# Kernel tuning notes

Measured on AMD Instinct MI355X. Metric: run time of the kernel, lower is better.

Reference implementation:

```python
import jax, jax.numpy as jnp
import numpy as np

# Dimensions
BATCH, L, DM = 4, 2048, 768          # batch, seq_len, d_model
EXPAND, DS, DC = 2, 16, 4            # expand, d_state, d_conv (mamba defaults)
DI = EXPAND * DM                     # d_inner = 1536
DTR = DM // 16                       # dt_rank = 48


def setup_inputs() -> dict:
    key = jax.random.key(0)
    ks = jax.random.split(key, 8)
    g = lambda k, shp, s=0.02: (jax.random.normal(k, shp, jnp.float32) * s)
    inputs = {
        "input": jax.random.normal(ks[0], (BATCH, L, DM), jnp.float32),
        "ln_w": jnp.ones((DM,), jnp.float32),
        "ln_b": jnp.zeros((DM,), jnp.float32),
        "W_in": g(ks[1], (2 * DI, DM)),            # in_proj weight (no bias)
        "conv_w": g(ks[2], (DI, 1, DC), 0.1),      # depthwise causal conv
        "conv_b": jnp.zeros((DI,), jnp.float32),
        "W_x": g(ks[3], (DTR + 2 * DS, DI)),       # x_proj -> (dt, B, C)
        "W_dt": g(ks[4], (DI, DTR)),               # dt_proj weight
        "b_dt": jnp.full((DI,), -4.0, jnp.float32),# dt_proj bias (small init dt)
        "A_log": jnp.log(jnp.broadcast_to(jnp.arange(1, DS + 1, dtype=jnp.float32), (DI, DS))),
        "D_ssm": jnp.ones((DI,), jnp.float32),
        "W_out": g(ks[5], (DM, DI)),               # out_proj (no bias)
    }
    return inputs


def _mamba_forward(input, ln_w, ln_b, W_in, conv_w, conv_b, W_x, W_dt, b_dt, A_log, D_ssm, W_out):
    skip = input
    # LayerNorm over last dim
    mu = jnp.mean(input, axis=-1, keepdims=True)
    var = jnp.var(input, axis=-1, keepdims=True)
    xn = (input - mu) * jax.lax.rsqrt(var + 1e-5) * ln_w + ln_b

    # in_proj -> x, z  (B, L, 2*DI)
    xz = jnp.einsum("bld,ed->ble", xn, W_in)
    x, z = jnp.split(xz, 2, axis=-1)

    # depthwise causal conv1d along L, then SiLU
    xc = jnp.transpose(x, (0, 2, 1))  # (B, DI, L)
    xc = jax.lax.conv_general_dilated(
        xc, conv_w, window_strides=(1,), padding=[(DC - 1, 0)],
        feature_group_count=conv_w.shape[0],
        dimension_numbers=("NCH", "OIH", "NCH"))
    xc = xc + conv_b[None, :, None]
    u = jax.nn.silu(jnp.transpose(xc, (0, 2, 1)))  # (B, L, DI)

    # x_proj -> dt, Bmat, Cmat
    dbc = jnp.einsum("bld,ed->ble", u, W_x)
    dt_rank = W_dt.shape[1]
    d_state = A_log.shape[1]
    dt = dbc[..., :dt_rank]
    Bm = dbc[..., dt_rank:dt_rank + d_state]   # (B, L, DS)
    Cm = dbc[..., dt_rank + d_state:]          # (B, L, DS)

    delta = jax.nn.softplus(jnp.einsum("blr,dr->bld", dt, W_dt) + b_dt)  # (B, L, DI)
    A = -jnp.exp(A_log)  # (DI, DS)

    def step(h, inp):
        d_t, B_t, C_t, u_t = inp  # (B,DI),(B,DS),(B,DS),(B,DI)
        dA = jnp.exp(d_t[..., None] * A)                       # (B, DI, DS)
        h = dA * h + (d_t * u_t)[..., None] * B_t[:, None, :]  # (B, DI, DS)
        y_t = jnp.einsum("bds,bs->bd", h, C_t)
        return h, y_t

    h0 = jnp.zeros((u.shape[0], A.shape[0], d_state), u.dtype)
    xs = (jnp.swapaxes(delta, 0, 1), jnp.swapaxes(Bm, 0, 1),
          jnp.swapaxes(Cm, 0, 1), jnp.swapaxes(u, 0, 1))
    _, ys = jax.lax.scan(step, h0, xs)
    y = jnp.swapaxes(ys, 0, 1) + u * D_ssm  # (B, L, DI)

    y = y * jax.nn.silu(z)
    out = jnp.einsum("ble,de->bld", y, W_out)
    return out + skip


def reference(input, ln_w, ln_b, W_in, conv_w, conv_b, W_x, W_dt, b_dt, A_log, D_ssm, W_out):
    return _mamba_forward(input, ln_w, ln_b, W_in, conv_w, conv_b, W_x, W_dt, b_dt, A_log, D_ssm, W_out)
```

## Files before the change

### kernel.cpp

```cpp
#include <hip/hip_runtime.h>
#include <math.h>

#define BATCH 4
#define SEQL  2048
#define DM    768
#define DI    1536
#define DS    16
#define DTR   48
#define NXZ   3072
#define NDBC  80
#define MROWS (BATCH*SEQL)
#define CHUNK 32
#define NC    (SEQL/CHUNK)

typedef __bf16 bf16x8 __attribute__((ext_vector_type(8)));
typedef float  f32x4  __attribute__((ext_vector_type(4)));
typedef float  f32x2  __attribute__((ext_vector_type(2)));
typedef unsigned short u16x8 __attribute__((ext_vector_type(8)));

__device__ __forceinline__ unsigned short f2bf(float f) {
    unsigned int u = __float_as_uint(f);
    unsigned int r = u + 0x7fffu + ((u >> 16) & 1u);
    return (unsigned short)(r >> 16);
}
__device__ __forceinline__ float bf2f(unsigned short u) {
    return __uint_as_float((unsigned int)u << 16);
}

__device__ __forceinline__ void gload16(const unsigned short* g, unsigned short* l) {
    __builtin_amdgcn_global_load_lds(
        (const __attribute__((address_space(1))) unsigned int*)g,
        (__attribute__((address_space(3))) unsigned int*)l,
        16, 0, 0);
}

#define VM_WAIT(n) asm volatile("s_waitcnt vmcnt(" #n ")" ::: "memory")
#define LGKM_WAIT0() asm volatile("s_waitcnt lgkmcnt(0)" ::: "memory")
#define RAW_BAR() asm volatile("s_barrier" ::: "memory")

__global__ __launch_bounds__(256) void convert_all(const float* __restrict__ W_in,
                                                   const float* __restrict__ W_x,
                                                   const float* __restrict__ W_out,
                                                   const float* __restrict__ W_dt,
                                                   unsigned short* __restrict__ Win_bf,
                                                   unsigned short* __restrict__ Wx_bf,
                                                   unsigned short* __restrict__ Wout_bf,
                                                   unsigned short* __restrict__ Wdt_bf)
{
    int bid = blockIdx.x, tid = threadIdx.x;
    const float* in; unsigned short* out; int i;
    if (bid < 2304)      { in = W_in;  out = Win_bf;  i = bid * 256 + tid;          if (i >= 589824) return; }
    else if (bid < 2424) { in = W_x;   out = Wx_bf;   i = (bid - 2304) * 256 + tid; if (i >= 30720)  return; }
    else if (bid < 3576) { in = W_out; out = Wout_bf; i = (bid - 2424) * 256 + tid; if (i >= 294912) return; }
    else {
        int j = (bid - 3576) * 256 + tid;
        int n = j >> 6, k = j & 63;
        Wdt_bf[j] = (k < 48) ? f2bf(W_dt[n * 48 + k]) : (unsigned short)0;
        return;
    }
    float4 v = *reinterpret_cast<const float4*>(in + (size_t)i * 4);
    size_t o = (size_t)i * 4;
    out[o+0] = f2bf(v.x); out[o+1] = f2bf(v.y);
    out[o+2] = f2bf(v.z); out[o+3] = f2bf(v.w);
}

__global__ __launch_bounds__(192) void ln_kernel(const float* __restrict__ inp,
                                                 const float* __restrict__ w,
                                                 const float* __restrict__ b,
                                                 unsigned short* __restrict__ out)
{
    int row = blockIdx.x;
    const float* x = inp + (size_t)row * DM;
    unsigned short* o = out + (size_t)row * DM;
    int tid = threadIdx.x;

    float4 v = *reinterpret_cast<const float4*>(x + tid * 4);
    float s  = v.x + v.y + v.z + v.w;
    float sq = v.x*v.x + v.y*v.y + v.z*v.z + v.w*v.w;

    for (int off = 32; off > 0; off >>= 1) {
        s  += __shfl_down(s, off);
        sq += __shfl_down(sq, off);
    }
    __shared__ float sa[3], sb[3];
    int lane = tid & 63, wv = tid >> 6;
    if (lane == 0) { sa[wv] = s; sb[wv] = sq; }
    __syncthreads();
    float tot  = sa[0] + sa[1] + sa[2];
    float totq = sb[0] + sb[1] + sb[2];

    float mean = tot * (1.0f / DM);
    float var  = totq * (1.0f / DM) - mean * mean;
    float rstd = rsqrtf(var + 1e-5f);

    float4 wv4 = *reinterpret_cast<const float4*>(w + tid * 4);
    float4 bv4 = *reinterpret_cast<const float4*>(b + tid * 4);
    ushort4 o4;
    o4.x = f2bf((v.x - mean) * rstd * wv4.x + bv4.x);
    o4.y = f2bf((v.y - mean) * rstd * wv4.y + bv4.y);
    o4.z = f2bf((v.z - mean) * rstd * wv4.z + bv4.z);
    o4.w = f2bf((v.w - mean) * rstd * wv4.w + bv4.w);
    *reinterpret_cast<ushort4*>(o + tid * 4) = o4;
}

__global__ __launch_bounds__(512, 2) void gemm_256(const unsigned short* __restrict__ A,
                                                   const unsigned short* __restrict__ W,
                                                   unsigned short* __restrict__ C, int ldc,
                                                   int K)
{
    extern __shared__ unsigned short smem[];
    unsigned short* As0 = smem;
    unsigned short* Bs0 = smem + 2 * 16384;

    const int tid  = threadIdx.x;
    const int lane = tid & 63;
    const int w    = tid >> 6;
    const int wm   = w >> 2, wn = w & 3;

    const int flat = blockIdx.y * gridDim.x + blockIdx.x;
    const int cpx  = (gridDim.x * gridDim.y) >> 3;
    const int swz  = (flat & 7) * cpx + (flat >> 3);
    const int m0   = (swz / gridDim.x) * 256;
    const int n0   = (swz % gridDim.x) * 256;

    const int rq = lane >> 3;
    const int cbk = (lane & 7) ^ rq;
    const unsigned short* pA[4];
    const unsigned short* pB[4];
    #pragma unroll
    for (int i = 0; i < 4; ++i) {
        int row = (w * 4 + i) * 8 + rq;
        pA[i] = A + (size_t)(m0 + row) * K + cbk * 8;
        pB[i] = W + (size_t)(n0 + row) * K + cbk * 8;
    }

    const int lr  = lane & 15;
    const int ln4 = lane >> 4;

    f32x4 acc[8][4];
    #pragma unroll
    for (int f = 0; f < 8; ++f)
        #pragma unroll
        for (int g = 0; g < 4; ++g)
            acc[f][g] = (f32x4){0.f, 0.f, 0.f, 0.f};

    const int NT = K >> 6;

    auto STAGE = [&](int bufi, int kt) {
        #pragma unroll
        for (int i = 0; i < 4; ++i) {
            gload16(pA[i] + (size_t)kt * 64, &As0[bufi * 16384 + (w * 4 + i) * 512]);
            gload16(pB[i] + (size_t)kt * 64, &Bs0[bufi * 16384 + (w * 4 + i) * 512]);
        }
    };

    STAGE(0, 0);
    VM_WAIT(0);
    RAW_BAR();
    STAGE(1, 1);

    int cur = 0;
    for (int kt = 0; kt < NT; ++kt) {
        const unsigned short* Ab = &As0[cur * 16384];
        const unsigned short* Bb = &Bs0[cur * 16384];
        #pragma unroll
        for (int kk = 0; kk < 2; ++kk) {
            const int co = ((kk * 4 + ln4) ^ (lr & 7)) * 8;
            bf16x8 af[8], bfr[4];
            #pragma unroll
            for (int f = 0; f < 8; ++f)
                af[f] = *reinterpret_cast<const bf16x8*>(&Ab[(wm * 128 + f * 16 + lr) * 64 + co]);
            #pragma unroll
            for (int g = 0; g < 4; ++g)
                bfr[g] = *reinterpret_cast<const bf16x8*>(&Bb[(wn * 64 + g * 16 + lr) * 64 + co]);
            __builtin_amdgcn_s_setprio(1);
            #pragma unroll
            for (int f = 0; f < 8; ++f)
                #pragma unroll
                for (int g = 0; g < 4; ++g)
                    acc[f][g] = __builtin_amdgcn_mfma_f32_16x16x32_bf16(af[f], bfr[g], acc[f][g], 0, 0, 0);
            __builtin_amdgcn_s_setprio(0);
        }

        if (kt + 1 < NT) {
            LGKM_WAIT0();
            RAW_BAR();
            if (kt + 2 < NT) {
                STAGE(cur, kt + 2);
                VM_WAIT(8);
            } else {
                VM_WAIT(0);
            }
            RAW_BAR();
            cur ^= 1;
        }
    }

    const int cr = ln4 * 4;
    #pragma unroll
    for (int f = 0; f < 8; ++f) {
        int mbase = m0 + wm * 128 + f * 16 + cr;
        #pragma unroll
        for (int g = 0; g < 4; ++g) {
            int n = n0 + wn * 64 + g * 16 + lr;
            #pragma unroll
            for (int r = 0; r < 4; ++r)
                C[(size_t)(mbase + r) * ldc + n] = f2bf(acc[f][g][r]);
        }
    }
}

template<int EPI>
__global__ __launch_bounds__(256) void gemm_pipe(const unsigned short* __restrict__ A,
                                                 const unsigned short* __restrict__ W,
                                                 void* __restrict__ Cv, int ldc,
                                                 int K,
                                                 const float* __restrict__ skip)
{
    __shared__ unsigned short As[2][128 * 64];
    __shared__ unsigned short Bs[2][128 * 64];

    const int tid  = threadIdx.x;
    const int lane = tid & 63;
    const int wid  = tid >> 6;
    const int wr   = wid >> 1, wcn = wid & 1;

    const int flat = blockIdx.y * gridDim.x + blockIdx.x;
    const int cpx  = (gridDim.x * gridDim.y) >> 3;
    const int swz  = (flat & 7) * cpx + (flat >> 3);
    const int m0   = (swz / gridDim.x) * 128;
    const int n0   = (swz % gridDim.x) * 128;

    const int swz3 = (tid >> 3) & 7;
    const unsigned short* pA = A + (size_t)(m0 + (tid >> 3)) * K + ((tid & 7) ^ swz3) * 8;
    const unsigned short* pB = W + (size_t)(n0 + (tid >> 3)) * K + ((tid & 7) ^ swz3) * 8;

    const int lr   = lane & 15;
    const int ln4  = lane >> 4;
    const int swzA = lr & 7;
    const int aoff = (wr * 64 + lr) * 64;
    const int boff = (wcn * 64 + lr) * 64;
    const int co0  = (ln4 ^ swzA) * 8;
    const int co1  = ((4 + ln4) ^ swzA) * 8;

    f32x4 acc[4][4];
    #pragma unroll
    for (int i = 0; i < 4; ++i)
        #pragma unroll
        for (int j = 0; j < 4; ++j)
            acc[i][j] = (f32x4){0.f, 0.f, 0.f, 0.f};

    const int NT = K >> 6;

    auto STAGE = [&](int bufi, int kt) {
        const unsigned short* a = pA + (size_t)kt * 64;
        const unsigned short* b = pB + (size_t)kt * 64;
        #pragma unroll
        for (int i = 0; i < 4; ++i) {
            gload16(a + (size_t)i * 32 * K, &As[bufi][(i * 256 + wid * 64) * 8]);
            gload16(b + (size_t)i * 32 * K, &Bs[bufi][(i * 256 + wid * 64) * 8]);
        }
    };

    STAGE(0, 0);
    VM_WAIT(0);
    RAW_BAR();
    STAGE(1, 1);

    int cur = 0;
    for (int kt = 0; kt < NT; ++kt) {
        const unsigned short* Ab = &As[cur][0];
        const unsigned short* Bb = &Bs[cur][0];
        #pragma unroll
        for (int kk = 0; kk < 2; ++kk) {
            const int co = kk ? co1 : co0;
            bf16x8 af[4], bfr[4];
            #pragma unroll
            for (int i = 0; i < 4; ++i)
                af[i] = *reinterpret_cast<const bf16x8*>(&Ab[aoff + i * 1024 + co]);
            #pragma unroll
            for (int j = 0; j < 4; ++j)
                bfr[j] = *reinterpret_cast<const bf16x8*>(&Bb[boff + j * 1024 + co]);
            #pragma unroll
            for (int i = 0; i < 4; ++i)
                #pragma unroll
                for (int j = 0; j < 4; ++j)
                    acc[i][j] = __builtin_amdgcn_mfma_f32_16x16x32_bf16(af[i], bfr[j], acc[i][j], 0, 0, 0);
        }

        if (kt + 1 < NT) {
            LGKM_WAIT0();
            RAW_BAR();
            if (kt + 2 < NT) {
                STAGE(cur, kt + 2);
                VM_WAIT(8);
            } else {
                VM_WAIT(0);
            }
            RAW_BAR();
            cur ^= 1;
        }
    }

    const int cr = ln4 * 4, cc = lr;
    #pragma unroll
    for (int i = 0; i < 4; ++i) {
        int mbase = m0 + wr * 64 + i * 16 + cr;
        #pragma unroll
        for (int j = 0; j < 4; ++j) {
            int n = n0 + wcn * 64 + j * 16 + cc;
            #pragma unroll
            for (int r = 0; r < 4; ++r) {
                float v = acc[i][j][r];
                size_t off = (size_t)(mbase + r) * ldc + n;
                if constexpr (EPI == 0) {
                    ((unsigned short*)Cv)[off] = f2bf(v);
                } else {
                    ((float*)Cv)[off] = v + skip[off];
                }
            }
        }
    }
}

__global__ __launch_bounds__(256) void gemm_k64_sp(const unsigned short* __restrict__ A,
                                                   const unsigned short* __restrict__ W,
                                                   unsigned short* __restrict__ C,
                                                   const float* __restrict__ bias)
{
    __shared__ unsigned short As[128 * 64];
    __shared__ unsigned short Bs[128 * 64];

    const int tid  = threadIdx.x;
    const int lane = tid & 63;
    const int wid  = tid >> 6;
    const int wr   = wid >> 1, wcn = wid & 1;

    const int flat = blockIdx.y * gridDim.x + blockIdx.x;
    const int cpx  = (gridDim.x * gridDim.y) >> 3;
    const int swz  = (flat & 7) * cpx + (flat >> 3);
    const int m0   = (swz / gridDim.x) * 128;
    const int n0   = (swz % gridDim.x) * 128;

    const int swz3 = (tid >> 3) & 7;
    const unsigned short* pA = A + (size_t)(m0 + (tid >> 3)) * 64 + ((tid & 7) ^ swz3) * 8;
    const unsigned short* pB = W + (size_t)(n0 + (tid >> 3)) * 64 + ((tid & 7) ^ swz3) * 8;

    #pragma unroll
    for (int i = 0; i < 4; ++i) {
        gload16(pA + (size_t)i * 32 * 64, &As[(i * 256 + wid * 64) * 8]);
        gload16(pB + (size_t)i * 32 * 64, &Bs[(i * 256 + wid * 64) * 8]);
    }
    __syncthreads();

    const int lr   = lane & 15;
    const int ln4  = lane >> 4;
    const int swzA = lr & 7;
    const int aoff = (wr * 64 + lr) * 64;
    const int boff = (wcn * 64 + lr) * 64;
    const int co0  = (ln4 ^ swzA) * 8;
    const int co1  = ((4 + ln4) ^ swzA) * 8;

    f32x4 acc[4][4];
    #pragma unroll
    for (int i = 0; i < 4; ++i)
        #pragma unroll
        for (int j = 0; j < 4; ++j)
            acc[i][j] = (f32x4){0.f, 0.f, 0.f, 0.f};

    #pragma unroll
    for (int kk = 0; kk < 2; ++kk) {
        const int co = kk ? co1 : co0;
        bf16x8 af[4], bfr[4];
        #pragma unroll
        for (int i = 0; i < 4; ++i)
            af[i] = *reinterpret_cast<const bf16x8*>(&As[aoff + i * 1024 + co]);
        #pragma unroll
        for (int j = 0; j < 4; ++j)
            bfr[j] = *reinterpret_cast<const bf16x8*>(&Bs[boff + j * 1024 + co]);
        #pragma unroll
        for (int i = 0; i < 4; ++i)
            #pragma unroll
            for (int j = 0; j < 4; ++j)
                acc[i][j] = __builtin_amdgcn_mfma_f32_16x16x32_bf16(af[i], bfr[j], acc[i][j], 0, 0, 0);
    }

    const int cr = ln4 * 4, cc = lr;
    #pragma unroll
    for (int i = 0; i < 4; ++i) {
        int mbase = m0 + wr * 64 + i * 16 + cr;
        #pragma unroll
        for (int j = 0; j < 4; ++j) {
            int n = n0 + wcn * 64 + j * 16 + cc;
            float bb = bias[n];
            #pragma unroll
            for (int r = 0; r < 4; ++r) {
                float v = acc[i][j][r] + bb;
                v = (v > 20.f) ? v : log1pf(__expf(v));
                C[(size_t)(mbase + r) * DI + n] = f2bf(v);
            }
        }
    }
}

#define KS 384
__global__ __launch_bounds__(256) void gemm_dbc_k4(const unsigned short* __restrict__ A,
                                                   const unsigned short* __restrict__ W,
                                                   float* __restrict__ part)
{
    __shared__ unsigned short As[128 * 32];
    __shared__ unsigned short Bs[128 * 32];

    const int tid  = threadIdx.x;
    const int lane = tid & 63;
    const int w    = tid >> 6;
    const int wr   = w >> 1, wc = w & 1;
    const int kx   = blockIdx.x;
    const int m0   = blockIdx.y * 128;

    const int srow = tid >> 2;
    const int scb  = (tid & 3) ^ ((srow >> 1) & 3);
    const unsigned short* Ap0 = A + (size_t)(m0 + srow) * DI + kx * KS + scb * 8;
    const unsigned short* Ap1 = Ap0 + (size_t)64 * DI;
    int br0 = min(srow, NDBC - 1);
    int br1 = min(64 + srow, NDBC - 1);
    const unsigned short* Wp0 = W + (size_t)br0 * DI + kx * KS + scb * 8;
    const unsigned short* Wp1 = W + (size_t)br1 * DI + kx * KS + scb * 8;

    f32x4 acc[4][4];
    #pragma unroll
    for (int i = 0; i < 4; ++i)
        #pragma unroll
        for (int j = 0; j < 4; ++j)
            acc[i][j] = (f32x4){0.f, 0.f, 0.f, 0.f};

    const int lr = lane & 15;
    const int lk = (((lane >> 4) ^ ((lr >> 1) & 3))) * 8;

    for (int k0 = 0; k0 < KS; k0 += 32) {
        gload16(Ap0 + k0, &As[0] + w * 512);
        gload16(Ap1 + k0, &As[0] + 2048 + w * 512);
        gload16(Wp0 + k0, &Bs[0] + w * 512);
        gload16(Wp1 + k0, &Bs[0] + 2048 + w * 512);
        __syncthreads();

        bf16x8 af[4], bfr[4];
        #pragma unroll
        for (int i = 0; i < 4; ++i)
            af[i] = *reinterpret_cast<const bf16x8*>(&As[(wr*64 + i*16 + lr) * 32 + lk]);
        #pragma unroll
        for (int j = 0; j < 4; ++j)
            bfr[j] = *reinterpret_cast<const bf16x8*>(&Bs[(wc*64 + j*16 + lr) * 32 + lk]);

        #pragma unroll
        for (int i = 0; i < 4; ++i)
            #pragma unroll
            for (int j = 0; j < 4; ++j)
                acc[i][j] = __builtin_amdgcn_mfma_f32_16x16x32_bf16(af[i], bfr[j], acc[i][j], 0, 0, 0);
        __syncthreads();
    }

    const int cr = (lane >> 4) * 4, cc = lane & 15;
    float* out = part + (size_t)kx * MROWS * NDBC;
    #pragma unroll
    for (int i = 0; i < 4; ++i) {
        int mbase = m0 + wr*64 + i*16 + cr;
        #pragma unroll
        for (int j = 0; j < 4; ++j) {
            int n = wc*64 + j*16 + cc;
            if (n < NDBC) {
                #pragma unroll
                for (int r = 0; r < 4; ++r)
                    out[(size_t)(mbase + r) * NDBC + n] = acc[i][j][r];
            }
        }
    }
}

__global__ __launch_bounds__(256) void reduce_dbc(const float* __restrict__ part,
                                                  float* __restrict__ dbc,
                                                  unsigned short* __restrict__ dt_bf)
{
    int i = blockIdx.x * 256 + threadIdx.x;
    const size_t S = (size_t)MROWS * NDBC;
    float v = part[i] + part[i + S] + part[i + 2*S] + part[i + 3*S];
    dbc[i] = v;
    int col = i % NDBC, row = i / NDBC;
    if (col < 64)
        dt_bf[(size_t)row * 64 + col] = (col < 48) ? f2bf(v) : (unsigned short)0;
}

__global__ __launch_bounds__(256) void conv_silu8(const unsigned short* __restrict__ xz,
                                                  const float* __restrict__ cw,
                                                  const float* __restrict__ cb,
                                                  unsigned short* __restrict__ ubf)
{
    int g  = blockIdx.x * 256 + threadIdx.x;
    int d8 = (g % 192) * 8;
    int bl = g / 192;
    int t  = bl & (SEQL - 1);
    const unsigned short* base = xz + (size_t)bl * NXZ + d8;

    u16x8 x0 = {}, x1 = {}, x2 = {}, x3;
    if (t >= 3) x0 = *reinterpret_cast<const u16x8*>(base - 3 * NXZ);
    if (t >= 2) x1 = *reinterpret_cast<const u16x8*>(base - 2 * NXZ);
    if (t >= 1) x2 = *reinterpret_cast<const u16x8*>(base - 1 * NXZ);
    x3 = *reinterpret_cast<const u16x8*>(base);

    u16x8 res;
    #pragma unroll
    for (int c = 0; c < 8; ++c) {
        int d = d8 + c;
        const float4 wv = *reinterpret_cast<const float4*>(cw + d * 4);
        float acc = cb[d]
                  + wv.x * bf2f(x0[c]) + wv.y * bf2f(x1[c])
                  + wv.z * bf2f(x2[c]) + wv.w * bf2f(x3[c]);
        float s = acc / (1.f + __expf(-acc));
        res[c] = f2bf(s);
    }
    *reinterpret_cast<u16x8*>(ubf + (size_t)bl * DI + d8) = res;
}

__global__ __launch_bounds__(256) void scan_pass1(const unsigned short* __restrict__ delta,
                                                  const unsigned short* __restrict__ u,
                                                  const float* __restrict__ dbc,
                                                  float* __restrict__ Ssum,
                                                  float* __restrict__ Hc)
{
    __shared__ float sB[CHUNK][DS];
    int bc = blockIdx.x / 6;
    int dg = blockIdx.x % 6;
    int b = bc / NC, c = bc % NC;
    int d = dg * 256 + threadIdx.x;
    size_t rowbase = (size_t)b * SEQL + (size_t)c * CHUNK;

    for (int i = threadIdx.x; i < CHUNK * DS; i += 256) {
        int tl = i >> 4, col = i & 15;
        sB[tl][col] = dbc[(rowbase + tl) * NDBC + DTR + col];
    }
    __syncthreads();

    f32x2 h[8] = {};
    float ss = 0.f;
    size_t idx = rowbase * DI + d;

    #pragma unroll 4
    for (int t = 0; t < CHUNK; ++t, idx += DI) {
        float dlt = bf2f(delta[idx]);
        float du  = dlt * bf2f(u[idx]);
        ss += dlt;
        float e1 = __expf(-dlt);
        float e2 = e1*e1;
        f32x2 ep  = {e1, e2};
        f32x2 e2v = {e2, e2};
        f32x2 du2 = {du, du};
        const f32x2* Bv = reinterpret_cast<const f32x2*>(&sB[t][0]);
        #pragma unroll
        for (int p = 0; p < 8; ++p) {
            h[p] = ep * h[p] + du2 * Bv[p];
            ep *= e2v;
        }
    }
    Ssum[(size_t)bc * DI + d] = ss;
    #pragma unroll
    for (int p = 0; p < 8; ++p) {
        Hc[((size_t)bc * DS + 2*p    ) * DI + d] = h[p].x;
        Hc[((size_t)bc * DS + 2*p + 1) * DI + d] = h[p].y;
    }
}

__global__ __launch_bounds__(256) void scan_carry(const float* __restrict__ Ssum,
                                                  const float* __restrict__ Hc,
                                                  float* __restrict__ hinit)
{
    int bs = blockIdx.x / 6;
    int dg = blockIdx.x % 6;
    int b = bs / DS, s = bs % DS;
    int d = dg * 256 + threadIdx.x;
    float a = -(float)(s + 1);
    float h = 0.f;
    for (int c0 = 0; c0 < NC; c0 += 8) {
        float P[8], H[8];
        #pragma unroll
        for (int j = 0; j < 8; ++j) {
            size_t bc = (size_t)b * NC + c0 + j;
            P[j] = Ssum[bc * DI + d];
            H[j] = Hc[(bc * DS + s) * DI + d];
        }
        #pragma unroll
        for (int j = 0; j < 8; ++j) {
            size_t bc = (size_t)b * NC + c0 + j;
            hinit[(bc * DS + s) * DI + d] = h;
            h = __expf(a * P[j]) * h + H[j];
        }
    }
}

__global__ __launch_bounds__(256) void scan_pass2(const unsigned short* __restrict__ delta,
                                                  const unsigned short* __restrict__ u,
                                                  const float* __restrict__ dbc,
                                                  const unsigned short* __restrict__ xz,
                                                  const float* __restrict__ D_ssm,
                                                  const float* __restrict__ hinit,
                                                  unsigned short* __restrict__ ybf)
{
    __shared__ float sBC[CHUNK][32];
    int bc = blockIdx.x / 6;
    int dg = blockIdx.x % 6;
    int b = bc / NC, c = bc % NC;
    int d = dg * 256 + threadIdx.x;
    size_t rowbase = (size_t)b * SEQL + (size_t)c * CHUNK;

    for (int i = threadIdx.x; i < CHUNK * 32; i += 256) {
        int tl = i >> 5, col = i & 31;
        sBC[tl][col] = dbc[(rowbase + tl) * NDBC + DTR + col];
    }
    __syncthreads();

    f32x2 h[8];
    #pragma unroll
    for (int p = 0; p < 8; ++p) {
        h[p].x = hinit[((size_t)bc * DS + 2*p    ) * DI + d];
        h[p].y = hinit[((size_t)bc * DS + 2*p + 1) * DI + d];
    }
    float Dv = D_ssm[d];

    size_t idx  = rowbase * DI + d;
    size_t idxz = rowbase * NXZ + DI + d;

    #pragma unroll 2
    for (int t = 0; t < CHUNK; ++t, idx += DI, idxz += NXZ) {
        float dlt = bf2f(delta[idx]);
        float uv  = bf2f(u[idx]);
        float zv  = bf2f(xz[idxz]);
        float du  = dlt * uv;
        float e1 = __expf(-dlt);
        float e2 = e1*e1;
        f32x2 ep  = {e1, e2};
        f32x2 e2v = {e2, e2};
        f32x2 du2 = {du, du};
        const f32x2* Bv = reinterpret_cast<const f32x2*>(&sBC[t][0]);
        const f32x2* Cp = reinterpret_cast<const f32x2*>(&sBC[t][16]);
        f32x2 yv = {0.f, 0.f};
        #pragma unroll
        for (int p = 0; p < 8; ++p) {
            h[p] = ep * h[p] + du2 * Bv[p];
            yv   = yv + h[p] * Cp[p];
            ep *= e2v;
        }
        float y = yv.x + yv.y;
        y += uv * Dv;
        y *= zv / (1.f + __expf(-zv));
        ybf[idx] = f2bf(y);
    }
}

extern "C" void kernel_launch(void* const* d_in, const int* in_sizes, int n_in,
                              void* d_out, int out_size, void* d_ws, size_t ws_size,
                              hipStream_t stream)
{
    const float* input  = (const float*)d_in[0];
    const float* ln_w   = (const float*)d_in[1];
    const float* ln_b   = (const float*)d_in[2];
    const float* W_in   = (const float*)d_in[3];
    const float* conv_w = (const float*)d_in[4];
    const float* conv_b = (const float*)d_in[5];
    const float* W_x    = (const float*)d_in[6];
    const float* W_dt   = (const float*)d_in[7];
    const float* b_dt   = (const float*)d_in[8];
    const float* D_ssm  = (const float*)d_in[10];
    const float* W_out  = (const float*)d_in[11];
    float* out = (float*)d_out;

    char* wsb = (char*)d_ws;
    unsigned short* xz_bf    = (unsigned short*)(wsb);
    unsigned short* u_bf     = (unsigned short*)(wsb + 50331648);
    float*          dbc      = (float*)        (wsb + 75497472);
    unsigned short* delta_bf = (unsigned short*)(wsb + 78118912);
    unsigned short* y_bf     = (unsigned short*)(wsb + 103284736);
    unsigned short* xn_bf    = (unsigned short*)(wsb + 128450560);
    float*          Ssum     = (float*)        (wsb + 141033472);
    float*          Hc       = (float*)        (wsb + 142606336);
    float*          hinit    = (float*)        (wsb + 167772160);
    unsigned short* Win_bf   = (unsigned short*)(wsb + 192937984);
    unsigned short* Wx_bf    = (unsigned short*)(wsb + 197656576);
    unsigned short* Wout_bf  = (unsigned short*)(wsb + 197902336);
    unsigned short* dt_bf    = (unsigned short*)(wsb + 200261632);
    unsigned short* Wdt_bf   = (unsigned short*)(wsb + 201310208);
    float*          dbc_part = (float*)        (wsb + 201506816);

    static bool attr_set = false;
    if (!attr_set) {
        hipFuncSetAttribute((const void*)gemm_256,
                            hipFuncAttributeMaxDynamicSharedMemorySize, 131072);
        attr_set = true;
    }

    hipLaunchKernelGGL(convert_all, dim3(3960), dim3(256), 0, stream,
                       W_in, W_x, W_out, W_dt, Win_bf, Wx_bf, Wout_bf, Wdt_bf);

    hipLaunchKernelGGL(ln_kernel, dim3(MROWS), dim3(192), 0, stream, input, ln_w, ln_b, xn_bf);

    hipLaunchKernelGGL(gemm_256, dim3(NXZ/256, MROWS/256), dim3(512), 131072, stream,
                       xn_bf, Win_bf, xz_bf, NXZ, DM);

    hipLaunchKernelGGL(conv_silu8, dim3(MROWS * 192 / 256), dim3(256), 0, stream,
                       xz_bf, conv_w, conv_b, u_bf);

    hipLaunchKernelGGL(gemm_dbc_k4, dim3(4, MROWS/128), dim3(256), 0, stream,
                       u_bf, Wx_bf, dbc_part);
    hipLaunchKernelGGL(reduce_dbc, dim3(MROWS*NDBC/256), dim3(256), 0, stream,
                       dbc_part, dbc, dt_bf);

    hipLaunchKernelGGL(gemm_k64_sp, dim3(DI/128, MROWS/128), dim3(256), 0, stream,
                       dt_bf, Wdt_bf, delta_bf, b_dt);

    hipLaunchKernelGGL(scan_pass1, dim3(BATCH * NC * 6), dim3(256), 0, stream,
                       delta_bf, u_bf, dbc, Ssum, Hc);
    hipLaunchKernelGGL(scan_carry, dim3(BATCH * DS * 6), dim3(256), 0, stream,
                       Ssum, Hc, hinit);
    hipLaunchKernelGGL(scan_pass2, dim3(BATCH * NC * 6), dim3(256), 0, stream,
                       delta_bf, u_bf, dbc, xz_bf, D_ssm, hinit, y_bf);

    hipLaunchKernelGGL((gemm_pipe<2>), dim3(DM/128, MROWS/128), dim3(256), 0, stream,
                       y_bf, Wout_bf, out, DM, DI, input);
}
```

Baseline: 278.3 us.

## Restructure in_proj GEMM into four-phase ping-pong schedule with interleaved prefetch

```diff
diff --git a/kernel.cpp b/kernel.cpp
--- a/kernel.cpp
+++ b/kernel.cpp
@@ -103,14 +103,12 @@
     *reinterpret_cast<ushort4*>(o + tid * 4) = o4;
 }
 
-__global__ __launch_bounds__(512, 2) void gemm_256(const unsigned short* __restrict__ A,
-                                                   const unsigned short* __restrict__ W,
-                                                   unsigned short* __restrict__ C, int ldc,
-                                                   int K)
+__global__ __launch_bounds__(512, 2) void gemm_8p(const unsigned short* __restrict__ A,
+                                                  const unsigned short* __restrict__ W,
+                                                  unsigned short* __restrict__ C, int ldc,
+                                                  int K)
 {
     extern __shared__ unsigned short smem[];
-    unsigned short* As0 = smem;
-    unsigned short* Bs0 = smem + 2 * 16384;
 
     const int tid  = threadIdx.x;
     const int lane = tid & 63;
@@ -123,19 +121,10 @@
     const int m0   = (swz / gridDim.x) * 256;
     const int n0   = (swz % gridDim.x) * 256;
 
-    const int rq = lane >> 3;
-    const int cbk = (lane & 7) ^ rq;
-    const unsigned short* pA[4];
-    const unsigned short* pB[4];
-    #pragma unroll
-    for (int i = 0; i < 4; ++i) {
-        int row = (w * 4 + i) * 8 + rq;
-        pA[i] = A + (size_t)(m0 + row) * K + cbk * 8;
-        pB[i] = W + (size_t)(n0 + row) * K + cbk * 8;
-    }
-
-    const int lr  = lane & 15;
-    const int ln4 = lane >> 4;
+    const int rowoff = tid >> 3;
+    const int cbk    = (tid & 7) ^ ((tid >> 3) & 7);
+    const int lr = lane & 15, ln4 = lane >> 4;
+    const int sx = lr & 7;
 
     f32x4 acc[8][4];
     #pragma unroll
@@ -146,54 +135,101 @@
 
     const int NT = K >> 6;
 
-    auto STAGE = [&](int bufi, int kt) {
-        #pragma unroll
-        for (int i = 0; i < 4; ++i) {
-            gload16(pA[i] + (size_t)kt * 64, &As0[bufi * 16384 + (w * 4 + i) * 512]);
-            gload16(pB[i] + (size_t)kt * 64, &Bs0[bufi * 16384 + (w * 4 + i) * 512]);
-        }
+    auto STAGE = [&](int d, int which, int kt) {
+        const unsigned short* gp = (which < 2)
+            ? A + (size_t)(m0 + which * 128) * K
+            : W + (size_t)(n0 + (which - 2) * 128) * K;
+        gp += (size_t)rowoff * K + (size_t)kt * 64 + cbk * 8;
+        unsigned short* lp = smem + ((d << 2) + which) * 8192 + (w * 8) * 64;
+        gload16(gp, lp);
+        gload16(gp + (size_t)64 * K, lp + 64 * 64);
     };
 
-    STAGE(0, 0);
+    STAGE(0,0,0); STAGE(0,1,0); STAGE(0,2,0); STAGE(0,3,0);
     VM_WAIT(0);
     RAW_BAR();
-    STAGE(1, 1);
+
+    bf16x8 afl[4][2];
+    bf16x8 bfl[2][2][2];
 
     int cur = 0;
-    for (int kt = 0; kt < NT; ++kt) {
-        const unsigned short* Ab = &As0[cur * 16384];
-        const unsigned short* Bb = &Bs0[cur * 16384];
-        #pragma unroll
-        for (int kk = 0; kk < 2; ++kk) {
-            const int co = ((kk * 4 + ln4) ^ (lr & 7)) * 8;
-            bf16x8 af[8], bfr[4];
-            #pragma unroll
-            for (int f = 0; f < 8; ++f)
-                af[f] = *reinterpret_cast<const bf16x8*>(&Ab[(wm * 128 + f * 16 + lr) * 64 + co]);
-            #pragma unroll
-            for (int g = 0; g < 4; ++g)
-                bfr[g] = *reinterpret_cast<const bf16x8*>(&Bb[(wn * 64 + g * 16 + lr) * 64 + co]);
-            __builtin_amdgcn_s_setprio(1);
-            #pragma unroll
-            for (int f = 0; f < 8; ++f)
+    for (int t = 0; t < NT; ++t) {
+        const unsigned short* RA = smem + ((cur << 2) + wm) * 8192;
+        const unsigned short* RB = smem + ((cur << 2) + 2 + (wn >> 1)) * 8192;
+        const int rbb = (wn & 1) * 64;
+        const int nb = cur ^ 1;
+        const bool more = (t + 1 < NT);
+
+        #pragma unroll
+        for (int f = 0; f < 4; ++f)
+            #pragma unroll
+            for (int kk = 0; kk < 2; ++kk)
+                afl[f][kk] = *reinterpret_cast<const bf16x8*>(&RA[(f*16 + lr)*64 + ((kk*4 + ln4) ^ sx)*8]);
+        #pragma unroll
+        for (int g = 0; g < 2; ++g)
+            #pragma unroll
+            for (int kk = 0; kk < 2; ++kk)
+                bfl[0][g][kk] = *reinterpret_cast<const bf16x8*>(&RB[(rbb + g*16 + lr)*64 + ((kk*4 + ln4) ^ sx)*8]);
+        if (more) { STAGE(nb,0,t+1); STAGE(nb,1,t+1); STAGE(nb,2,t+1); }
+        RAW_BAR();
+        __builtin_amdgcn_s_setprio(1);
+        #pragma unroll
+        for (int f = 0; f < 4; ++f)
+            #pragma unroll
+            for (int g = 0; g < 2; ++g)
                 #pragma unroll
-                for (int g = 0; g < 4; ++g)
-                    acc[f][g] = __builtin_amdgcn_mfma_f32_16x16x32_bf16(af[f], bfr[g], acc[f][g], 0, 0, 0);
-            __builtin_amdgcn_s_setprio(0);
-        }
-
-        if (kt + 1 < NT) {
-            LGKM_WAIT0();
-            RAW_BAR();
-            if (kt + 2 < NT) {
-                STAGE(cur, kt + 2);
-                VM_WAIT(8);
-            } else {
-                VM_WAIT(0);
-            }
-            RAW_BAR();
-            cur ^= 1;
-        }
+                for (int kk = 0; kk < 2; ++kk)
+                    acc[f][g] = __builtin_amdgcn_mfma_f32_16x16x32_bf16(afl[f][kk], bfl[0][g][kk], acc[f][g], 0, 0, 0);
+        __builtin_amdgcn_s_setprio(0);
+        RAW_BAR();
+
+        #pragma unroll
+        for (int g = 0; g < 2; ++g)
+            #pragma unroll
+            for (int kk = 0; kk < 2; ++kk)
+                bfl[1][g][kk] = *reinterpret_cast<const bf16x8*>(&RB[(rbb + (2+g)*16 + lr)*64 + ((kk*4 + ln4) ^ sx)*8]);
+        if (more) STAGE(nb,3,t+1);
+        RAW_BAR();
+        __builtin_amdgcn_s_setprio(1);
+        #pragma unroll
+        for (int f = 0; f < 4; ++f)
+            #pragma unroll
+            for (int g = 0; g < 2; ++g)
+                #pragma unroll
+                for (int kk = 0; kk < 2; ++kk)
+                    acc[f][2+g] = __builtin_amdgcn_mfma_f32_16x16x32_bf16(afl[f][kk], bfl[1][g][kk], acc[f][2+g], 0, 0, 0);
+        __builtin_amdgcn_s_setprio(0);
+        RAW_BAR();
+
+        #pragma unroll
+        for (int f = 0; f < 4; ++f)
+            #pragma unroll
+            for (int kk = 0; kk < 2; ++kk)
+                afl[f][kk] = *reinterpret_cast<const bf16x8*>(&RA[((4+f)*16 + lr)*64 + ((kk*4 + ln4) ^ sx)*8]);
+        RAW_BAR();
+        __builtin_amdgcn_s_setprio(1);
+        #pragma unroll
+        for (int f = 0; f < 4; ++f)
+            #pragma unroll
+            for (int g = 0; g < 2; ++g)
+                #pragma unroll
+                for (int kk = 0; kk < 2; ++kk)
+                    acc[4+f][g] = __builtin_amdgcn_mfma_f32_16x16x32_bf16(afl[f][kk], bfl[0][g][kk], acc[4+f][g], 0, 0, 0);
+        __builtin_amdgcn_s_setprio(0);
+        RAW_BAR();
+
+        __builtin_amdgcn_s_setprio(1);
+        #pragma unroll
+        for (int f = 0; f < 4; ++f)
+            #pragma unroll
+            for (int g = 0; g < 2; ++g)
+                #pragma unroll
+                for (int kk = 0; kk < 2; ++kk)
+                    acc[4+f][2+g] = __builtin_amdgcn_mfma_f32_16x16x32_bf16(afl[f][kk], bfl[1][g][kk], acc[4+f][2+g], 0, 0, 0);
+        __builtin_amdgcn_s_setprio(0);
+        if (more) VM_WAIT(0);
+        RAW_BAR();
+        cur ^= 1;
     }
 
     const int cr = ln4 * 4;
@@ -691,7 +727,7 @@
 
     static bool attr_set = false;
     if (!attr_set) {
-        hipFuncSetAttribute((const void*)gemm_256,
+        hipFuncSetAttribute((const void*)gemm_8p,
                             hipFuncAttributeMaxDynamicSharedMemorySize, 131072);
         attr_set = true;
     }
@@ -701,7 +737,7 @@
 
     hipLaunchKernelGGL(ln_kernel, dim3(MROWS), dim3(192), 0, stream, input, ln_w, ln_b, xn_bf);
 
-    hipLaunchKernelGGL(gemm_256, dim3(NXZ/256, MROWS/256), dim3(512), 131072, stream,
+    hipLaunchKernelGGL(gemm_8p, dim3(NXZ/256, MROWS/256), dim3(512), 131072, stream,
                        xn_bf, Win_bf, xz_bf, NXZ, DM);
 
     hipLaunchKernelGGL(conv_silu8, dim3(MROWS * 192 / 256), dim3(256), 0, stream,
```

Result: no change. 275.7 us (-0.9%).

## Retile in_proj GEMM to 256x128 tiles and store scan carries in bf16

Applied to the files above, without the earlier changes.

```diff
diff --git a/kernel.cpp b/kernel.cpp
--- a/kernel.cpp
+++ b/kernel.cpp
@@ -103,55 +103,56 @@
     *reinterpret_cast<ushort4*>(o + tid * 4) = o4;
 }
 
-__global__ __launch_bounds__(512, 2) void gemm_256(const unsigned short* __restrict__ A,
-                                                   const unsigned short* __restrict__ W,
-                                                   unsigned short* __restrict__ C, int ldc,
-                                                   int K)
+__global__ __launch_bounds__(512, 2) void gemm_bigm(const unsigned short* __restrict__ A,
+                                                    const unsigned short* __restrict__ W,
+                                                    unsigned short* __restrict__ C, int ldc,
+                                                    int K)
 {
     extern __shared__ unsigned short smem[];
-    unsigned short* As0 = smem;
-    unsigned short* Bs0 = smem + 2 * 16384;
+    unsigned short* As = smem;
+    unsigned short* Bs = smem + 32768;
 
     const int tid  = threadIdx.x;
     const int lane = tid & 63;
     const int w    = tid >> 6;
-    const int wm   = w >> 2, wn = w & 3;
+    const int wm   = w >> 1, wn = w & 1;
 
     const int flat = blockIdx.y * gridDim.x + blockIdx.x;
     const int cpx  = (gridDim.x * gridDim.y) >> 3;
     const int swz  = (flat & 7) * cpx + (flat >> 3);
     const int m0   = (swz / gridDim.x) * 256;
-    const int n0   = (swz % gridDim.x) * 256;
-
-    const int rq = lane >> 3;
-    const int cbk = (lane & 7) ^ rq;
-    const unsigned short* pA[4];
-    const unsigned short* pB[4];
-    #pragma unroll
-    for (int i = 0; i < 4; ++i) {
-        int row = (w * 4 + i) * 8 + rq;
-        pA[i] = A + (size_t)(m0 + row) * K + cbk * 8;
-        pB[i] = W + (size_t)(n0 + row) * K + cbk * 8;
-    }
-
-    const int lr  = lane & 15;
-    const int ln4 = lane >> 4;
-
-    f32x4 acc[8][4];
-    #pragma unroll
-    for (int f = 0; f < 8; ++f)
-        #pragma unroll
-        for (int g = 0; g < 4; ++g)
-            acc[f][g] = (f32x4){0.f, 0.f, 0.f, 0.f};
+    const int n0   = (swz % gridDim.x) * 128;
+
+    const int srow = tid >> 3;
+    const int scb  = (tid & 7) ^ (srow & 7);
+    const unsigned short* pA = A + (size_t)(m0 + srow) * K + scb * 8;
+    const unsigned short* pB = W + (size_t)(n0 + srow) * K + scb * 8;
+
+    const int lr = lane & 15, ln4 = lane >> 4;
+    const int sx = lr & 7;
+    const int co0 = (ln4 ^ sx) * 8;
+    const int co1 = ((4 + ln4) ^ sx) * 8;
+    const int aoff = (wm * 64 + lr) * 64;
+    const int boff = (wn * 64 + lr) * 64;
+
+    f32x4 acc[4][4];
+    #pragma unroll
+    for (int i = 0; i < 4; ++i)
+        #pragma unroll
+        for (int j = 0; j < 4; ++j)
+            acc[i][j] = (f32x4){0.f, 0.f, 0.f, 0.f};
 
     const int NT = K >> 6;
 
     auto STAGE = [&](int bufi, int kt) {
-        #pragma unroll
-        for (int i = 0; i < 4; ++i) {
-            gload16(pA[i] + (size_t)kt * 64, &As0[bufi * 16384 + (w * 4 + i) * 512]);
-            gload16(pB[i] + (size_t)kt * 64, &Bs0[bufi * 16384 + (w * 4 + i) * 512]);
-        }
+        const unsigned short* a = pA + (size_t)kt * 64;
+        const unsigned short* b = pB + (size_t)kt * 64;
+        #pragma unroll
+        for (int i = 0; i < 4; ++i)
+            gload16(a + (size_t)i * 64 * K, &As[bufi * 16384 + (i * 512 + tid) * 8]);
+        #pragma unroll
+        for (int i = 0; i < 2; ++i)
+            gload16(b + (size_t)i * 64 * K, &Bs[bufi * 8192 + (i * 512 + tid) * 8]);
     };
 
     STAGE(0, 0);
@@ -161,25 +162,131 @@
 
     int cur = 0;
     for (int kt = 0; kt < NT; ++kt) {
-        const unsigned short* Ab = &As0[cur * 16384];
-        const unsigned short* Bb = &Bs0[cur * 16384];
+        const unsigned short* Ab = &As[cur * 16384];
+        const unsigned short* Bb = &Bs[cur * 8192];
         #pragma unroll
         for (int kk = 0; kk < 2; ++kk) {
-            const int co = ((kk * 4 + ln4) ^ (lr & 7)) * 8;
-            bf16x8 af[8], bfr[4];
-            #pragma unroll
-            for (int f = 0; f < 8; ++f)
-                af[f] = *reinterpret_cast<const bf16x8*>(&Ab[(wm * 128 + f * 16 + lr) * 64 + co]);
-            #pragma unroll
-            for (int g = 0; g < 4; ++g)
-                bfr[g] = *reinterpret_cast<const bf16x8*>(&Bb[(wn * 64 + g * 16 + lr) * 64 + co]);
+            const int co = kk ? co1 : co0;
+            bf16x8 af[4], bfr[4];
+            #pragma unroll
+            for (int i = 0; i < 4; ++i)
+                af[i] = *reinterpret_cast<const bf16x8*>(&Ab[aoff + i * 1024 + co]);
+            #pragma unroll
+            for (int j = 0; j < 4; ++j)
+                bfr[j] = *reinterpret_cast<const bf16x8*>(&Bb[boff + j * 1024 + co]);
             __builtin_amdgcn_s_setprio(1);
             #pragma unroll
-            for (int f = 0; f < 8; ++f)
+            for (int i = 0; i < 4; ++i)
                 #pragma unroll
-                for (int g = 0; g < 4; ++g)
-                    acc[f][g] = __builtin_amdgcn_mfma_f32_16x16x32_bf16(af[f], bfr[g], acc[f][g], 0, 0, 0);
+                for (int j = 0; j < 4; ++j)
+                    acc[i][j] = __builtin_amdgcn_mfma_f32_16x16x32_bf16(af[i], bfr[j], acc[i][j], 0, 0, 0);
             __builtin_amdgcn_s_setprio(0);
+        }
+
+        if (kt + 1 < NT) {
+            LGKM_WAIT0();
+            RAW_BAR();
+            if (kt + 2 < NT) {
+                STAGE(cur, kt + 2);
+                VM_WAIT(6);
+            } else {
+                VM_WAIT(0);
+            }
+            RAW_BAR();
+            cur ^= 1;
+        }
+    }
+
+    const int cr = ln4 * 4;
+    #pragma unroll
+    for (int i = 0; i < 4; ++i) {
+        int mbase = m0 + wm * 64 + i * 16 + cr;
+        #pragma unroll
+        for (int j = 0; j < 4; ++j) {
+            int n = n0 + wn * 64 + j * 16 + lr;
+            #pragma unroll
+            for (int r = 0; r < 4; ++r)
+                C[(size_t)(mbase + r) * ldc + n] = f2bf(acc[i][j][r]);
+        }
+    }
+}
+
+template<int EPI>
+__global__ __launch_bounds__(256) void gemm_pipe(const unsigned short* __restrict__ A,
+                                                 const unsigned short* __restrict__ W,
+                                                 void* __restrict__ Cv, int ldc,
+                                                 int K,
+                                                 const float* __restrict__ skip)
+{
+    __shared__ unsigned short As[2][128 * 64];
+    __shared__ unsigned short Bs[2][128 * 64];
+
+    const int tid  = threadIdx.x;
+    const int lane = tid & 63;
+    const int wid  = tid >> 6;
+    const int wr   = wid >> 1, wcn = wid & 1;
+
+    const int flat = blockIdx.y * gridDim.x + blockIdx.x;
+    const int cpx  = (gridDim.x * gridDim.y) >> 3;
+    const int swz  = (flat & 7) * cpx + (flat >> 3);
+    const int m0   = (swz / gridDim.x) * 128;
+    const int n0   = (swz % gridDim.x) * 128;
+
+    const int swz3 = (tid >> 3) & 7;
+    const unsigned short* pA = A + (size_t)(m0 + (tid >> 3)) * K + ((tid & 7) ^ swz3) * 8;
+    const unsigned short* pB = W + (size_t)(n0 + (tid >> 3)) * K + ((tid & 7) ^ swz3) * 8;
+
+    const int lr   = lane & 15;
+    const int ln4  = lane >> 4;
+    const int swzA = lr & 7;
+    const int aoff = (wr * 64 + lr) * 64;
+    const int boff = (wcn * 64 + lr) * 64;
+    const int co0  = (ln4 ^ swzA) * 8;
+    const int co1  = ((4 + ln4) ^ swzA) * 8;
+
+    f32x4 acc[4][4];
+    #pragma unroll
+    for (int i = 0; i < 4; ++i)
+        #pragma unroll
+        for (int j = 0; j < 4; ++j)
+            acc[i][j] = (f32x4){0.f, 0.f, 0.f, 0.f};
+
+    const int NT = K >> 6;
+
+    auto STAGE = [&](int bufi, int kt) {
+        const unsigned short* a = pA + (size_t)kt * 64;
+        const unsigned short* b = pB + (size_t)kt * 64;
+        #pragma unroll
+        for (int i = 0; i < 4; ++i) {
+            gload16(a + (size_t)i * 32 * K, &As[bufi][(i * 256 + wid * 64) * 8]);
+            gload16(b + (size_t)i * 32 * K, &Bs[bufi][(i * 256 + wid * 64) * 8]);
+        }
+    };
+
+    STAGE(0, 0);
+    VM_WAIT(0);
+    RAW_BAR();
+    STAGE(1, 1);
+
+    int cur = 0;
+    for (int kt = 0; kt < NT; ++kt) {
+        const unsigned short* Ab = &As[cur][0];
+        const unsigned short* Bb = &Bs[cur][0];
+        #pragma unroll
+        for (int kk = 0; kk < 2; ++kk) {
+            const int co = kk ? co1 : co0;
+            bf16x8 af[4], bfr[4];
+            #pragma unroll
+            for (int i = 0; i < 4; ++i)
+                af[i] = *reinterpret_cast<const bf16x8*>(&Ab[aoff + i * 1024 + co]);
+            #pragma unroll
+            for (int j = 0; j < 4; ++j)
+                bfr[j] = *reinterpret_cast<const bf16x8*>(&Bb[boff + j * 1024 + co]);
+            #pragma unroll
+            for (int i = 0; i < 4; ++i)
+                #pragma unroll
+                for (int j = 0; j < 4; ++j)
+                    acc[i][j] = __builtin_amdgcn_mfma_f32_16x16x32_bf16(af[i], bfr[j], acc[i][j], 0, 0, 0);
         }
 
         if (kt + 1 < NT) {
@@ -196,112 +303,6 @@
         }
     }
 
-    const int cr = ln4 * 4;
-    #pragma unroll
-    for (int f = 0; f < 8; ++f) {
-        int mbase = m0 + wm * 128 + f * 16 + cr;
-        #pragma unroll
-        for (int g = 0; g < 4; ++g) {
-            int n = n0 + wn * 64 + g * 16 + lr;
-            #pragma unroll
-            for (int r = 0; r < 4; ++r)
-                C[(size_t)(mbase + r) * ldc + n] = f2bf(acc[f][g][r]);
-        }
-    }
-}
-
-template<int EPI>
-__global__ __launch_bounds__(256) void gemm_pipe(const unsigned short* __restrict__ A,
-                                                 const unsigned short* __restrict__ W,
-                                                 void* __restrict__ Cv, int ldc,
-                                                 int K,
-                                                 const float* __restrict__ skip)
-{
-    __shared__ unsigned short As[2][128 * 64];
-    __shared__ unsigned short Bs[2][128 * 64];
-
-    const int tid  = threadIdx.x;
-    const int lane = tid & 63;
-    const int wid  = tid >> 6;
-    const int wr   = wid >> 1, wcn = wid & 1;
-
-    const int flat = blockIdx.y * gridDim.x + blockIdx.x;
-    const int cpx  = (gridDim.x * gridDim.y) >> 3;
-    const int swz  = (flat & 7) * cpx + (flat >> 3);
-    const int m0   = (swz / gridDim.x) * 128;
-    const int n0   = (swz % gridDim.x) * 128;
-
-    const int swz3 = (tid >> 3) & 7;
-    const unsigned short* pA = A + (size_t)(m0 + (tid >> 3)) * K + ((tid & 7) ^ swz3) * 8;
-    const unsigned short* pB = W + (size_t)(n0 + (tid >> 3)) * K + ((tid & 7) ^ swz3) * 8;
-
-    const int lr   = lane & 15;
-    const int ln4  = lane >> 4;
-    const int swzA = lr & 7;
-    const int aoff = (wr * 64 + lr) * 64;
-    const int boff = (wcn * 64 + lr) * 64;
-    const int co0  = (ln4 ^ swzA) * 8;
-    const int co1  = ((4 + ln4) ^ swzA) * 8;
-
-    f32x4 acc[4][4];
-    #pragma unroll
-    for (int i = 0; i < 4; ++i)
-        #pragma unroll
-        for (int j = 0; j < 4; ++j)
-            acc[i][j] = (f32x4){0.f, 0.f, 0.f, 0.f};
-
-    const int NT = K >> 6;
-
-    auto STAGE = [&](int bufi, int kt) {
-        const unsigned short* a = pA + (size_t)kt * 64;
-        const unsigned short* b = pB + (size_t)kt * 64;
-        #pragma unroll
-        for (int i = 0; i < 4; ++i) {
-            gload16(a + (size_t)i * 32 * K, &As[bufi][(i * 256 + wid * 64) * 8]);
-            gload16(b + (size_t)i * 32 * K, &Bs[bufi][(i * 256 + wid * 64) * 8]);
-        }
-    };
-
-    STAGE(0, 0);
-    VM_WAIT(0);
-    RAW_BAR();
-    STAGE(1, 1);
-
-    int cur = 0;
-    for (int kt = 0; kt < NT; ++kt) {
-        const unsigned short* Ab = &As[cur][0];
-        const unsigned short* Bb = &Bs[cur][0];
-        #pragma unroll
-        for (int kk = 0; kk < 2; ++kk) {
-            const int co = kk ? co1 : co0;
-            bf16x8 af[4], bfr[4];
-            #pragma unroll
-            for (int i = 0; i < 4; ++i)
-                af[i] = *reinterpret_cast<const bf16x8*>(&Ab[aoff + i * 1024 + co]);
-            #pragma unroll
-            for (int j = 0; j < 4; ++j)
-                bfr[j] = *reinterpret_cast<const bf16x8*>(&Bb[boff + j * 1024 + co]);
-            #pragma unroll
-            for (int i = 0; i < 4; ++i)
-                #pragma unroll
-                for (int j = 0; j < 4; ++j)
-                    acc[i][j] = __builtin_amdgcn_mfma_f32_16x16x32_bf16(af[i], bfr[j], acc[i][j], 0, 0, 0);
-        }
-
-        if (kt + 1 < NT) {
-            LGKM_WAIT0();
-            RAW_BAR();
-            if (kt + 2 < NT) {
-                STAGE(cur, kt + 2);
-                VM_WAIT(8);
-            } else {
-                VM_WAIT(0);
-            }
-            RAW_BAR();
-            cur ^= 1;
-        }
-    }
-
     const int cr = ln4 * 4, cc = lr;
     #pragma unroll
     for (int i = 0; i < 4; ++i) {
@@ -525,7 +526,7 @@
                                                   const unsigned short* __restrict__ u,
                                                   const float* __restrict__ dbc,
                                                   float* __restrict__ Ssum,
-                                                  float* __restrict__ Hc)
+                                                  unsigned short* __restrict__ Hc)
 {
     __shared__ float sB[CHUNK][DS];
     int bc = blockIdx.x / 6;
@@ -564,14 +565,14 @@
     Ssum[(size_t)bc * DI + d] = ss;
     #pragma unroll
     for (int p = 0; p < 8; ++p) {
-        Hc[((size_t)bc * DS + 2*p    ) * DI + d] = h[p].x;
-        Hc[((size_t)bc * DS + 2*p + 1) * DI + d] = h[p].y;
+        Hc[((size_t)bc * DS + 2*p    ) * DI + d] = f2bf(h[p].x);
+        Hc[((size_t)bc * DS + 2*p + 1) * DI + d] = f2bf(h[p].y);
     }
 }
 
 __global__ __launch_bounds__(256) void scan_carry(const float* __restrict__ Ssum,
-                                                  const float* __restrict__ Hc,
-                                                  float* __restrict__ hinit)
+                                                  const unsigned short* __restrict__ Hc,
+                                                  unsigned short* __restrict__ hinit)
 {
     int bs = blockIdx.x / 6;
     int dg = blockIdx.x % 6;
@@ -585,12 +586,12 @@
         for (int j = 0; j < 8; ++j) {
             size_t bc = (size_t)b * NC + c0 + j;
             P[j] = Ssum[bc * DI + d];
-            H[j] = Hc[(bc * DS + s) * DI + d];
+            H[j] = bf2f(Hc[(bc * DS + s) * DI + d]);
         }
         #pragma unroll
         for (int j = 0; j < 8; ++j) {
             size_t bc = (size_t)b * NC + c0 + j;
-            hinit[(bc * DS + s) * DI + d] = h;
+            hinit[(bc * DS + s) * DI + d] = f2bf(h);
             h = __expf(a * P[j]) * h + H[j];
         }
     }
@@ -601,7 +602,7 @@
                                                   const float* __restrict__ dbc,
                                                   const unsigned short* __restrict__ xz,
                                                   const float* __restrict__ D_ssm,
-                                                  const float* __restrict__ hinit,
+                                                  const unsigned short* __restrict__ hinit,
                                                   unsigned short* __restrict__ ybf)
 {
     __shared__ float sBC[CHUNK][32];
@@ -620,8 +621,8 @@
     f32x2 h[8];
     #pragma unroll
     for (int p = 0; p < 8; ++p) {
-        h[p].x = hinit[((size_t)bc * DS + 2*p    ) * DI + d];
-        h[p].y = hinit[((size_t)bc * DS + 2*p + 1) * DI + d];
+        h[p].x = bf2f(hinit[((size_t)bc * DS + 2*p    ) * DI + d]);
+        h[p].y = bf2f(hinit[((size_t)bc * DS + 2*p + 1) * DI + d]);
     }
     float Dv = D_ssm[d];
 
@@ -680,19 +681,19 @@
     unsigned short* y_bf     = (unsigned short*)(wsb + 103284736);
     unsigned short* xn_bf    = (unsigned short*)(wsb + 128450560);
     float*          Ssum     = (float*)        (wsb + 141033472);
-    float*          Hc       = (float*)        (wsb + 142606336);
-    float*          hinit    = (float*)        (wsb + 167772160);
-    unsigned short* Win_bf   = (unsigned short*)(wsb + 192937984);
-    unsigned short* Wx_bf    = (unsigned short*)(wsb + 197656576);
-    unsigned short* Wout_bf  = (unsigned short*)(wsb + 197902336);
-    unsigned short* dt_bf    = (unsigned short*)(wsb + 200261632);
-    unsigned short* Wdt_bf   = (unsigned short*)(wsb + 201310208);
-    float*          dbc_part = (float*)        (wsb + 201506816);
+    unsigned short* Hc       = (unsigned short*)(wsb + 142606336);
+    unsigned short* hinit    = (unsigned short*)(wsb + 155189248);
+    unsigned short* Win_bf   = (unsigned short*)(wsb + 167772160);
+    unsigned short* Wx_bf    = (unsigned short*)(wsb + 172490752);
+    unsigned short* Wout_bf  = (unsigned short*)(wsb + 172736512);
+    unsigned short* dt_bf    = (unsigned short*)(wsb + 175095808);
+    unsigned short* Wdt_bf   = (unsigned short*)(wsb + 176144384);
+    float*          dbc_part = (float*)        (wsb + 176340992);
 
     static bool attr_set = false;
     if (!attr_set) {
-        hipFuncSetAttribute((const void*)gemm_256,
-                            hipFuncAttributeMaxDynamicSharedMemorySize, 131072);
+        hipFuncSetAttribute((const void*)gemm_bigm,
+                            hipFuncAttributeMaxDynamicSharedMemorySize, 98304);
         attr_set = true;
     }
 
@@ -701,7 +702,7 @@
 
     hipLaunchKernelGGL(ln_kernel, dim3(MROWS), dim3(192), 0, stream, input, ln_w, ln_b, xn_bf);
 
-    hipLaunchKernelGGL(gemm_256, dim3(NXZ/256, MROWS/256), dim3(512), 131072, stream,
+    hipLaunchKernelGGL(gemm_bigm, dim3(NXZ/128, MROWS/256), dim3(512), 98304, stream,
                        xn_bf, Win_bf, xz_bf, NXZ, DM);
 
     hipLaunchKernelGGL(conv_silu8, dim3(MROWS * 192 / 256), dim3(256), 0, stream,
```

New measurement: 260.0 us. 1.07x faster.
